# Performance work log

Hardware: AMD Instinct MI355X
Metric: run time of the kernel (lower is better)

The kernel has to match this reference:

```python
import jax, jax.numpy as jnp
import numpy as np

COST_CLASS, COST_BBOX, COST_GIOU = 2.0, 5.0, 2.0
ALPHA, GAMMA, EPS = 0.25, 2.0, 1e-8


def box_cxcywh_to_xyxy(x):
    cx, cy, w, h = x[..., 0], x[..., 1], x[..., 2], x[..., 3]
    return jnp.stack([cx - 0.5 * w, cy - 0.5 * h, cx + 0.5 * w, cy + 0.5 * h], axis=-1)


def pairwise_giou(b1, b2):
    # b1: [N,4] xyxy, b2: [M,4] xyxy -> [N,M]
    area1 = (b1[:, 2] - b1[:, 0]) * (b1[:, 3] - b1[:, 1])
    area2 = (b2[:, 2] - b2[:, 0]) * (b2[:, 3] - b2[:, 1])
    lt = jnp.maximum(b1[:, None, :2], b2[None, :, :2])   # [N,M,2]
    rb = jnp.minimum(b1[:, None, 2:], b2[None, :, 2:])
    wh = jnp.clip(rb - lt, 0.0)
    inter = wh[..., 0] * wh[..., 1]
    union = area1[:, None] + area2[None, :] - inter
    iou = inter / union
    lt2 = jnp.minimum(b1[:, None, :2], b2[None, :, :2])
    rb2 = jnp.maximum(b1[:, None, 2:], b2[None, :, 2:])
    wh2 = jnp.clip(rb2 - lt2, 0.0)
    area = wh2[..., 0] * wh2[..., 1]  # enclosing box area
    return iou - (area - union) / area


def setup_inputs() -> dict:
    key = jax.random.key(0)
    k1, k2, k3, k4 = jax.random.split(key, 4)
    bs, Q, C, T = 16, 900, 91, 1600
    return {
        "pred_logits": jax.random.normal(k1, (bs, Q, C), dtype=jnp.float32),
        "pred_boxes": jax.random.uniform(k2, (bs, Q, 4), dtype=jnp.float32),
        "tgt_boxes": jax.random.uniform(k3, (T, 4), dtype=jnp.float32),
        "tgt_ids": jax.random.randint(k4, (T,), 0, C),
    }


def reference(pred_logits, pred_boxes, tgt_boxes, tgt_ids):
    bs, Q, _ = pred_logits.shape
    out_prob = jax.nn.sigmoid(pred_logits.reshape(bs * Q, -1))  # [N, num_classes]
    out_bbox = pred_boxes.reshape(bs * Q, 4)                     # [N, 4] cxcywh

    # focal-style classification cost
    neg_cost = (1.0 - ALPHA) * out_prob ** GAMMA * (-jnp.log(1.0 - out_prob + EPS))
    pos_cost = ALPHA * (1.0 - out_prob) ** GAMMA * (-jnp.log(out_prob + EPS))
    cost_class = pos_cost[:, tgt_ids] - neg_cost[:, tgt_ids]     # [N, T]

    # L1 bbox cost (cdist p=1)
    cost_bbox = jnp.sum(jnp.abs(out_bbox[:, None, :] - tgt_boxes[None, :, :]), axis=-1)

    # GIoU cost
    cost_giou = -pairwise_giou(box_cxcywh_to_xyxy(out_bbox), box_cxcywh_to_xyxy(tgt_boxes))

    C = COST_BBOX * cost_bbox + COST_CLASS * cost_class + COST_GIOU * cost_giou
    return C.reshape(bs, Q, -1)
```

## Files before the change

kernel.cpp:

```cpp
#include <hip/hip_runtime.h>

#define F_ALPHA 0.25f
#define F_EPS   1e-8f
#define NB 4

__global__ void __launch_bounds__(256)
fused_cost_kernel(const float* __restrict__ logits,
                  const float4* __restrict__ pred_boxes,
                  const float4* __restrict__ tgt_boxes,
                  const int* __restrict__ tgt_ids,
                  float* __restrict__ out,
                  int N, int C, int T) {
    __shared__ float fcls[NB][96];
    const int n0  = blockIdx.x * NB;
    const int tid = threadIdx.x;

    {
        const int w = tid >> 6, l = tid & 63;
        const int n = min(n0 + w, N - 1);
        const float* lrow = logits + (size_t)n * C;
        for (int c = l; c < C; c += 64) {
            float x = lrow[c];
            float p = 1.0f / (1.0f + expf(-x));
            float om = 1.0f - p;
            float pos = F_ALPHA * om * om * (-logf(p + F_EPS));
            float neg = (1.0f - F_ALPHA) * p * p * (-logf(om + F_EPS));
            fcls[w][c] = 2.0f * (pos - neg) + 2.0f;
        }
    }

    float pcx[NB], pcy[NB], pw_[NB], ph_[NB];
    float px1[NB], py1[NB], px2[NB], py2[NB], parea[NB];
    float* op[NB];
#pragma unroll
    for (int i = 0; i < NB; ++i) {
        const int n = min(n0 + i, N - 1);
        float4 pb = pred_boxes[n];
        pcx[i] = pb.x; pcy[i] = pb.y; pw_[i] = pb.z; ph_[i] = pb.w;
        px1[i] = pb.x - 0.5f * pb.z;  py1[i] = pb.y - 0.5f * pb.w;
        px2[i] = pb.x + 0.5f * pb.z;  py2[i] = pb.y + 0.5f * pb.w;
        parea[i] = pb.z * pb.w;
        op[i] = out + (size_t)n * T;
    }
    __syncthreads();

    auto body = [&](int t) {
        float4 tb = tgt_boxes[t];
        int id = tgt_ids[t];
        float tx1 = tb.x - 0.5f * tb.z, ty1 = tb.y - 0.5f * tb.w;
        float tx2 = tb.x + 0.5f * tb.z, ty2 = tb.y + 0.5f * tb.w;
        float tarea = tb.z * tb.w;
#pragma unroll
        for (int i = 0; i < NB; ++i) {
            float cls2 = fcls[i][id];

            float l1 = (fabsf(pcx[i] - tb.x) + fabsf(pcy[i] - tb.y))
                     + (fabsf(pw_[i] - tb.z) + fabsf(ph_[i] - tb.w));

            float ix1 = fmaxf(px1[i], tx1), iy1 = fmaxf(py1[i], ty1);
            float ix2 = fminf(px2[i], tx2), iy2 = fminf(py2[i], ty2);
            float iw = fmaxf(ix2 - ix1, 0.0f), ih = fmaxf(iy2 - iy1, 0.0f);
            float inter = iw * ih;
            float uni = parea[i] + tarea - inter;

            float ex1 = fminf(px1[i], tx1), ey1 = fminf(py1[i], ty1);
            float ex2 = fmaxf(px2[i], tx2), ey2 = fmaxf(py2[i], ty2);
            float earea = (ex2 - ex1) * (ey2 - ey1);

            float v = fmaf(5.0f, l1, cls2);
            v = fmaf(-2.0f, inter * __builtin_amdgcn_rcpf(uni), v);
            v = fmaf(-2.0f, uni * __builtin_amdgcn_rcpf(earea), v);
            op[i][t] = v;
        }
    };

    int t = tid;
    for (; t + 256 < T; t += 512) { body(t); body(t + 256); }
    for (; t < T; t += 256) body(t);
}

extern "C" void kernel_launch(void* const* d_in, const int* in_sizes, int n_in,
                              void* d_out, int out_size, void* d_ws, size_t ws_size,
                              hipStream_t stream) {
    const float* logits = (const float*)d_in[0];
    const float* pboxes = (const float*)d_in[1];
    const float* tboxes = (const float*)d_in[2];
    const int*   tids   = (const int*)d_in[3];

    int N = in_sizes[1] / 4;
    int C = in_sizes[0] / N;
    int T = in_sizes[2] / 4;

    int grid = (N + NB - 1) / NB;
    fused_cost_kernel<<<grid, 256, 0, stream>>>(
        logits, (const float4*)pboxes, (const float4*)tboxes, tids,
        (float*)d_out, N, C, T);
}
```

Measured before the change: 32.94 us.

## Stage targets in LDS, double rows per block, transpose class-cost table

Each block now handles 8 prediction rows instead of 4, halving the grid and doubling reuse of each target box. All target boxes and ids are copied into shared memory once per block, and the class-cost table is stored class-major so one target's 8 costs sit next to each other. The boundary clamps are removed, which assumes N is divisible by 8 and T is at most 1600. The bigger shared footprint (about 35 KB) and more registers may lower occupancy.

```diff
diff --git a/kernel.cpp b/kernel.cpp
--- a/kernel.cpp
+++ b/kernel.cpp
@@ -2,7 +2,8 @@
 
 #define F_ALPHA 0.25f
 #define F_EPS   1e-8f
-#define NB 4
+#define NB 8
+#define TMAX 1600
 
 __global__ void __launch_bounds__(256)
 fused_cost_kernel(const float* __restrict__ logits,
@@ -11,22 +12,26 @@
                   const int* __restrict__ tgt_ids,
                   float* __restrict__ out,
                   int N, int C, int T) {
-    __shared__ float fcls[NB][96];
+    __shared__ float4 sTb[TMAX];
+    __shared__ int    sId[TMAX];
+    __shared__ float  fclsT[96 * NB];
+
     const int n0  = blockIdx.x * NB;
     const int tid = threadIdx.x;
 
-    {
-        const int w = tid >> 6, l = tid & 63;
-        const int n = min(n0 + w, N - 1);
-        const float* lrow = logits + (size_t)n * C;
-        for (int c = l; c < C; c += 64) {
-            float x = lrow[c];
-            float p = 1.0f / (1.0f + expf(-x));
-            float om = 1.0f - p;
-            float pos = F_ALPHA * om * om * (-logf(p + F_EPS));
-            float neg = (1.0f - F_ALPHA) * p * p * (-logf(om + F_EPS));
-            fcls[w][c] = 2.0f * (pos - neg) + 2.0f;
-        }
+    for (int j = tid; j < T; j += 256) {
+        sTb[j] = tgt_boxes[j];
+        sId[j] = tgt_ids[j];
+    }
+
+    for (int k = tid; k < NB * C; k += 256) {
+        int i = k / C, c = k - i * C;
+        float x = logits[(size_t)(n0 + i) * C + c];
+        float p = 1.0f / (1.0f + expf(-x));
+        float om = 1.0f - p;
+        float pos = F_ALPHA * om * om * (-logf(p + F_EPS));
+        float neg = (1.0f - F_ALPHA) * p * p * (-logf(om + F_EPS));
+        fclsT[c * NB + i] = 2.0f * (pos - neg) + 2.0f;
     }
 
     float pcx[NB], pcy[NB], pw_[NB], ph_[NB];
@@ -34,7 +39,7 @@
     float* op[NB];
 #pragma unroll
     for (int i = 0; i < NB; ++i) {
-        const int n = min(n0 + i, N - 1);
+        const int n = n0 + i;
         float4 pb = pred_boxes[n];
         pcx[i] = pb.x; pcy[i] = pb.y; pw_[i] = pb.z; ph_[i] = pb.w;
         px1[i] = pb.x - 0.5f * pb.z;  py1[i] = pb.y - 0.5f * pb.w;
@@ -44,16 +49,17 @@
     }
     __syncthreads();
 
-    auto body = [&](int t) {
-        float4 tb = tgt_boxes[t];
-        int id = tgt_ids[t];
+    for (int t = tid; t < T; t += 256) {
+        float4 tb = sTb[t];
+        int id = sId[t];
+        const float* cls8 = &fclsT[id * NB];
+
         float tx1 = tb.x - 0.5f * tb.z, ty1 = tb.y - 0.5f * tb.w;
         float tx2 = tb.x + 0.5f * tb.z, ty2 = tb.y + 0.5f * tb.w;
         float tarea = tb.z * tb.w;
+
 #pragma unroll
         for (int i = 0; i < NB; ++i) {
-            float cls2 = fcls[i][id];
-
             float l1 = (fabsf(pcx[i] - tb.x) + fabsf(pcy[i] - tb.y))
                      + (fabsf(pw_[i] - tb.z) + fabsf(ph_[i] - tb.w));
 
@@ -67,16 +73,12 @@
             float ex2 = fmaxf(px2[i], tx2), ey2 = fmaxf(py2[i], ty2);
             float earea = (ex2 - ex1) * (ey2 - ey1);
 
-            float v = fmaf(5.0f, l1, cls2);
+            float v = fmaf(5.0f, l1, cls8[i]);
             v = fmaf(-2.0f, inter * __builtin_amdgcn_rcpf(uni), v);
             v = fmaf(-2.0f, uni * __builtin_amdgcn_rcpf(earea), v);
             op[i][t] = v;
         }
-    };
-
-    int t = tid;
-    for (; t + 256 < T; t += 512) { body(t); body(t + 256); }
-    for (; t < T; t += 256) body(t);
+    }
 }
 
 extern "C" void kernel_launch(void* const* d_in, const int* in_sizes, int n_in,
@@ -91,7 +93,7 @@
     int C = in_sizes[0] / N;
     int T = in_sizes[2] / 4;
 
-    int grid = (N + NB - 1) / NB;
+    int grid = N / NB;
     fused_cost_kernel<<<grid, 256, 0, stream>>>(
         logits, (const float4*)pboxes, (const float4*)tboxes, tids,
         (float*)d_out, N, C, T);
```

New measurement: 36.37 us. 10.4% more time.
